# Kernel tuning notes

Measured on AMD Instinct MI355X. Metric: run time of the kernel, lower is better.

## Reference

```python
import jax, jax.numpy as jnp
import numpy as np

B, S, D = 128, 256, 768          # batch, seq (pre-sentinel), encoder dim
ARC, TAG = 500, 100              # arc / tag representation dims
LAYERS, TOPK = 2, 8              # config['gnn_layers'], config['top_k']
SP = S + 1                       # seq_len after head sentinel


def setup_inputs() -> dict:
    key = jax.random.key(0)
    ks = jax.random.split(key, 32)
    sc = 0.02
    inp = {
        'inputs': jax.random.normal(ks[0], (B, S, D), jnp.float32),
        'tag_embeddings': jax.random.randint(ks[1], (B, S), 0, 50),
        'mask': jnp.ones((B, S), jnp.int32),
        'head_indices': jax.random.randint(ks[2], (B, S), 0, S),
        'head_tags': jax.random.randint(ks[3], (B, S), 0, 50),
        # parameters
        'head_sentinel': jax.random.normal(ks[4], (D,), jnp.float32),
        'W_ha': jax.random.normal(ks[5], (D, ARC)) * sc, 'b_ha': jnp.zeros((ARC,)),
        'W_da': jax.random.normal(ks[6], (D, ARC)) * sc, 'b_da': jnp.zeros((ARC,)),
        'W_ht': jax.random.normal(ks[7], (D, TAG)) * sc, 'b_ht': jnp.zeros((TAG,)),
        'W_dt': jax.random.normal(ks[8], (D, TAG)) * sc, 'b_dt': jnp.zeros((TAG,)),
        # bilinear attention: use_input_biases=True -> (ARC+1, ARC+1), plus scalar bias
        'bil_W': jax.random.normal(ks[9], (LAYERS + 1, ARC + 1, ARC + 1)) * sc,
        'bil_b': jnp.zeros((LAYERS + 1,)),
        # GCNConv params (PyG: x @ W, symmetric-normalized aggregate, + bias)
        'c1a_W': jax.random.normal(ks[10], (ARC, ARC)) * sc, 'c1a_b': jnp.zeros((ARC,)),
        'c2a_W': jax.random.normal(ks[11], (ARC, ARC)) * sc, 'c2a_b': jnp.zeros((ARC,)),
        'c1r_W': jax.random.normal(ks[12], (TAG, TAG)) * sc, 'c1r_b': jnp.zeros((TAG,)),
        'c2r_W': jax.random.normal(ks[13], (TAG, TAG)) * sc, 'c2r_b': jnp.zeros((TAG,)),
    }
    return inp


def bilinear_attn(m1, m2, W, b):
    # AllenNLP BilinearMatrixAttention with use_input_biases=True
    ones1 = jnp.ones(m1.shape[:-1] + (1,), m1.dtype)
    m1b = jnp.concatenate([m1, ones1], -1)
    m2b = jnp.concatenate([m2, ones1], -1)
    return jnp.einsum('bie,ef,bjf->bij', m1b, W, m2b) + b


def batch_top_k(probs, k):
    # probs: [B, SP, SP] row-softmaxed; edge j(head)->i(dep) for each row's top-k cols,
    # with global (batched) node indexing.
    vals, idx = jax.lax.top_k(probs, k)                      # [B, SP, k]
    offs = (jnp.arange(B) * SP)[:, None, None]
    src = (idx + offs).reshape(-1)
    dst = (jnp.broadcast_to(jnp.arange(SP)[None, :, None], idx.shape) + offs).reshape(-1)
    return src, dst, vals.reshape(-1)


def gcn_conv(x, src, dst, ew, W, b):
    # PyG GCNConv: x@W, add self-loops (weight 1), sym norm, scatter-add at dst, + bias
    N = x.shape[0]
    x = x @ W
    loop = jnp.arange(N)
    row = jnp.concatenate([src, loop])
    col = jnp.concatenate([dst, loop])
    w = jnp.concatenate([ew, jnp.ones((N,), x.dtype)])
    deg = jax.ops.segment_sum(w, col, num_segments=N)
    dinv = jnp.where(deg > 0, jax.lax.rsqrt(deg), 0.0)
    norm = dinv[row] * w * dinv[col]
    out = jax.ops.segment_sum(x[row] * norm[:, None], col, num_segments=N)
    return out + b


def reference(inputs, tag_embeddings, mask, head_indices, head_tags,
              head_sentinel, W_ha, b_ha, W_da, b_da, W_ht, b_ht, W_dt, b_dt,
              bil_W, bil_b, c1a_W, c1a_b, c2a_W, c2a_b, c1r_W, c1r_b, c2r_W, c2r_b):
    elu = jax.nn.elu
    x = jnp.concatenate([jnp.broadcast_to(head_sentinel, (B, 1, D)), inputs], axis=1)  # [B,SP,D]
    head_arc = elu(x @ W_ha + b_ha)
    dept_arc = elu(x @ W_da + b_da)
    head_tag = elu(x @ W_ht + b_ht)
    dep_tag = elu(x @ W_dt + b_dt)

    def two_conv(feat, W1, b1, W2, b2, src, dst, ew):
        h = gcn_conv(feat.reshape(B * SP, -1), src, dst, ew, W1, b1)
        h = gcn_conv(elu(h), src, dst, ew, W2, b2)
        return h.reshape(B, SP, -1)

    for k in range(LAYERS):
        arc_logits = bilinear_attn(head_arc, dept_arc, bil_W[k], bil_b[k])
        arc_probs = jax.nn.softmax(arc_logits, axis=-1)
        src, dst, ew = batch_top_k(arc_probs, TOPK)
        head_arc = two_conv(head_arc, c1a_W, c1a_b, c2a_W, c2a_b, src, dst, ew)
        dept_arc = two_conv(dept_arc, c1a_W, c1a_b, c2a_W, c2a_b, src, dst, ew)
        head_tag = two_conv(head_tag, c1r_W, c1r_b, c2r_W, c2r_b, src, dst, ew)
        dep_tag = two_conv(dep_tag, c1r_W, c1r_b, c2r_W, c2r_b, src, dst, ew)

    arc_logits = bilinear_attn(head_arc, dept_arc, bil_W[-1], bil_b[-1])
    return arc_logits, head_tag, dep_tag
```

## Files before the change

### kernel.cpp

```cpp
#include <hip/hip_runtime.h>
#include <hip/hip_bf16.h>
#include <math.h>
#include <cstddef>

namespace {

constexpr int kB   = 128;
constexpr int kS   = 256;
constexpr int kD   = 768;
constexpr int kSP  = 257;
constexpr int kN   = kB * kSP;
constexpr int kARC = 500;
constexpr int kTAG = 100;
constexpr int KA   = 512;
constexpr int KT   = 128;
constexpr int NPA  = 1024;
constexpr int NPT  = 256;

typedef __attribute__((ext_vector_type(8))) short short8;
typedef __attribute__((ext_vector_type(4))) float floatx4;
typedef __attribute__((ext_vector_type(2))) float floatx2;
typedef __attribute__((ext_vector_type(4))) unsigned short ushort4v;
typedef __attribute__((ext_vector_type(2))) unsigned short ushort2v;
typedef __hip_bfloat16 bf;

__device__ __forceinline__ float bfval(bf h) { return __bfloat162float(h); }
__device__ __forceinline__ unsigned short bfbits(bf h) {
  unsigned short u; __builtin_memcpy(&u, &h, 2); return u;
}
__device__ __forceinline__ void splitf(float x, bf* h, bf* l) {
  bf hh = __float2bfloat16(x);
  *h = hh;
  *l = __float2bfloat16(x - __bfloat162float(hh));
}

__device__ __forceinline__ int swz8(int lid, int total) {
  int q = total >> 3, r = total & 7;
  int c = lid & 7, p = lid >> 3;
  return (c < r ? c * (q + 1) : r * (q + 1) + (c - r) * q) + p;
}

__device__ __forceinline__ void gload16(const bf* g, bf* l) {
  __builtin_amdgcn_global_load_lds(
      (const __attribute__((address_space(1))) void*)g,
      (__attribute__((address_space(3))) void*)l, 16, 0, 0);
}

__global__ void zerofill(unsigned* __restrict__ p, long n4) {
  long i = (long)blockIdx.x * 256 + threadIdx.x;
  if (i < n4) p[i] = 0u;
}

__global__ void detect_dtype_n(const unsigned* __restrict__ raw, int* __restrict__ flag,
                               int nwords) {
  int lane = threadIdx.x;
  int ok = 0, nz = 0;
  if (lane < nwords) {
    unsigned w = raw[lane];
    if (w != 0u) {
      nz = 1;
      int e = (w >> 7) & 0xFF;
      ok = (e >= 90 && e <= 140);
    }
  }
  unsigned long long ball_ok = __ballot(ok);
  unsigned long long ball_nz = __ballot(nz);
  if (lane == 0) {
    int cok = __popcll(ball_ok), cnz = __popcll(ball_nz);
    flag[0] = (cok * 4 >= cnz * 3) ? 1 : 0;
  }
}

__device__ __forceinline__ float rawload(const void* p, size_t i, int bfm) {
  return bfm ? __bfloat162float(((const bf*)p)[i]) : ((const float*)p)[i];
}

__global__ void conv_off(const void* __restrict__ src, float* __restrict__ dst,
                         int n, long off, const int* __restrict__ flag) {
  int i = blockIdx.x * 256 + threadIdx.x;
  if (i >= n) return;
  dst[i] = rawload(src, (size_t)off + i, *flag);
}

__global__ void wsplit_t(const void* __restrict__ src, const int* __restrict__ flag,
                         long srcOff, int ldsrc, int K, int N, int Kpad,
                         bf* __restrict__ Wh, bf* __restrict__ Wl) {
  long idx = (long)blockIdx.x * 256 + threadIdx.x;
  if (idx >= (long)N * Kpad) return;
  int n = (int)(idx / Kpad), k = (int)(idx % Kpad);
  float v = (k < K) ? rawload(src, (size_t)srcOff + (size_t)k * ldsrc + n, *flag) : 0.f;
  bf h, l;
  splitf(v, &h, &l);
  Wh[idx] = h; Wl[idx] = l;
}

__global__ void xsplit(const void* __restrict__ inp, const void* __restrict__ sent,
                       const int* __restrict__ fi, const int* __restrict__ fs,
                       bf* __restrict__ xh, bf* __restrict__ xl, int g0, int NG) {
  long idx = (long)blockIdx.x * 256 + threadIdx.x;
  long tot = (long)NG * (kD / 4);
  if (idx >= tot) return;
  int n = (int)(idx / (kD / 4));
  int k = (int)(idx % (kD / 4)) * 4;
  int b = n / kSP, r = n - b * kSP;
  const void* src;
  size_t base;
  int bfm;
  if (r == 0) { src = sent; base = (size_t)k; bfm = *fs; }
  else {
    src = inp;
    base = ((size_t)((g0 + b) * kS + (r - 1))) * kD + k;
    bfm = *fi;
  }
  float v[4];
  if (bfm) {
    ushort4v s = *(const ushort4v*)((const unsigned short*)src + base);
#pragma unroll
    for (int j = 0; j < 4; ++j) {
      bf h; unsigned short u = s[j];
      __builtin_memcpy(&h, &u, 2);
      v[j] = __bfloat162float(h);
    }
  } else {
    floatx4 f4 = *(const floatx4*)((const float*)src + base);
#pragma unroll
    for (int j = 0; j < 4; ++j) v[j] = f4[j];
  }
  ushort4v h4, l4;
#pragma unroll
  for (int j = 0; j < 4; ++j) {
    bf h, l;
    splitf(v[j], &h, &l);
    h4[j] = bfbits(h); l4[j] = bfbits(l);
  }
  size_t o = (size_t)n * kD + k;
  *(ushort4v*)((unsigned short*)xh + o) = h4;
  *(ushort4v*)((unsigned short*)xl + o) = l4;
}

constexpr int BM = 128, BN = 128, BK = 32;

template <int EPI, int OUTF32>
__global__ __launch_bounds__(256) void gemm_sp(
    const bf* __restrict__ Ah, const bf* __restrict__ Al, int lda,
    const bf* __restrict__ Bh, const bf* __restrict__ Bl, int ldb,
    bf* __restrict__ Ch, bf* __restrict__ Cl, float* __restrict__ Cf, int ldc,
    int M, int N, int K, const float* __restrict__ bias) {
  __shared__ bf sAh[2][BM][BK];
  __shared__ bf sAl[2][BM][BK];
  __shared__ bf sBh[2][BN][BK];
  __shared__ bf sBl[2][BN][BK];
  const int tid = threadIdx.x;
  const int lane = tid & 63, wave = tid >> 6;
  const int quad = lane >> 4, l15 = lane & 15;
  const int wm = (wave >> 1) * 64, wn = (wave & 1) * 64;
  const int gy = gridDim.y;
  const int sw = swz8(blockIdx.x + blockIdx.y * gridDim.x, gridDim.x * gy);
  const int m0 = (sw / gy) * BM, n0 = (sw % gy) * BN;
  const int lrow = lane >> 2, lkof = (lane & 3) * 8;

  const bf *pAh[2], *pAl[2], *pBh[2], *pBl[2];
  int rb[2];
#pragma unroll
  for (int jj = 0; jj < 2; ++jj) {
    rb[jj] = wave * 32 + jj * 16;
    int gm = m0 + rb[jj] + lrow; if (gm > M - 1) gm = M - 1;
    int gn = n0 + rb[jj] + lrow; if (gn > N - 1) gn = N - 1;
    pAh[jj] = Ah + (size_t)gm * lda + lkof;
    pAl[jj] = Al + (size_t)gm * lda + lkof;
    pBh[jj] = Bh + (size_t)gn * ldb + lkof;
    pBl[jj] = Bl + (size_t)gn * ldb + lkof;
  }

  auto stage = [&](int bi, int k0) {
#pragma unroll
    for (int jj = 0; jj < 2; ++jj) {
      gload16(pAh[jj] + k0, &sAh[bi][rb[jj]][0]);
      gload16(pAl[jj] + k0, &sAl[bi][rb[jj]][0]);
      gload16(pBh[jj] + k0, &sBh[bi][rb[jj]][0]);
      gload16(pBl[jj] + k0, &sBl[bi][rb[jj]][0]);
    }
  };

  floatx4 acc[4][4] = {};
  stage(0, 0);
  int cur = 0;
  for (int k0 = 0; k0 < K; k0 += BK) {
    __syncthreads();
    if (k0 + BK < K) stage(cur ^ 1, k0 + BK);
    short8 a_h[4], a_l[4], b_h[4], b_l[4];
#pragma unroll
    for (int t = 0; t < 4; ++t) {
      a_h[t] = *(const short8*)&sAh[cur][wm + t * 16 + l15][quad * 8];
      a_l[t] = *(const short8*)&sAl[cur][wm + t * 16 + l15][quad * 8];
      b_h[t] = *(const short8*)&sBh[cur][wn + t * 16 + l15][quad * 8];
      b_l[t] = *(const short8*)&sBl[cur][wn + t * 16 + l15][quad * 8];
    }
#pragma unroll
    for (int mt = 0; mt < 4; ++mt)
#pragma unroll
      for (int nt = 0; nt < 4; ++nt) {
        acc[mt][nt] = __builtin_amdgcn_mfma_f32_16x16x32_bf16(a_h[mt], b_h[nt], acc[mt][nt], 0, 0, 0);
        acc[mt][nt] = __builtin_amdgcn_mfma_f32_16x16x32_bf16(a_h[mt], b_l[nt], acc[mt][nt], 0, 0, 0);
        acc[mt][nt] = __builtin_amdgcn_mfma_f32_16x16x32_bf16(a_l[mt], b_h[nt], acc[mt][nt], 0, 0, 0);
      }
    cur ^= 1;
  }
#pragma unroll
  for (int mt = 0; mt < 4; ++mt)
#pragma unroll
    for (int reg = 0; reg < 4; ++reg) {
      int m = m0 + wm + mt * 16 + quad * 4 + reg;
      if (m >= M) continue;
#pragma unroll
      for (int nt = 0; nt < 4; ++nt) {
        int n = n0 + wn + nt * 16 + l15;
        if (OUTF32) {
          if (n < N) {
            float v = acc[mt][nt][reg];
            if (EPI >= 1) v += bias[n];
            if (EPI == 1) v = v > 0.f ? v : expm1f(v);
            Cf[(size_t)m * ldc + n] = v;
          }
        } else {
          size_t o = (size_t)m * ldc + n;
          if (n < N) {
            float v = acc[mt][nt][reg];
            if (EPI >= 1) v += bias[n];
            if (EPI == 1) v = v > 0.f ? v : expm1f(v);
            bf h, l;
            splitf(v, &h, &l);
            Ch[o] = h; Cl[o] = l;
          } else if (n < ldc) {
            Ch[o] = __float2bfloat16(0.f);
            Cl[o] = __float2bfloat16(0.f);
          }
        }
      }
    }
}

__global__ __launch_bounds__(256) void bilnt_sp(
    const bf* __restrict__ Th, const bf* __restrict__ Tl,
    const bf* __restrict__ Fh, const bf* __restrict__ Fl, int ldf,
    float* __restrict__ out, const float* __restrict__ bilb, int bidx,
    int g0, int globOut) {
  __shared__ bf sAh[2][BM][BK];
  __shared__ bf sAl[2][BM][BK];
  __shared__ bf sBh[2][BN][BK];
  __shared__ bf sBl[2][BN][BK];
  const int tid = threadIdx.x;
  const int lane = tid & 63, wave = tid >> 6;
  const int quad = lane >> 4, l15 = lane & 15;
  const int wm = (wave >> 1) * 64, wn = (wave & 1) * 64;
  const int gx = gridDim.x, gxy = gridDim.x * gridDim.y;
  const int sw = swz8(blockIdx.x + gx * blockIdx.y + gxy * blockIdx.z, gxy * gridDim.z);
  const int z = sw / gxy;
  const int rem = sw % gxy;
  const int m0 = (rem % gx) * BM, n0 = (rem / gx) * BN;
  const int lrow = lane >> 2, lkof = (lane & 3) * 8;
  const bf* Ah = Th + (size_t)z * kSP * KA;
  const bf* Al = Tl + (size_t)z * kSP * KA;
  const bf* Bh = Fh + (size_t)z * kSP * ldf;
  const bf* Bl = Fl + (size_t)z * kSP * ldf;

  const bf *pAh[2], *pAl[2], *pBh[2], *pBl[2];
  int rb[2];
#pragma unroll
  for (int jj = 0; jj < 2; ++jj) {
    rb[jj] = wave * 32 + jj * 16;
    int gm = m0 + rb[jj] + lrow; if (gm > kSP - 1) gm = kSP - 1;
    int gn = n0 + rb[jj] + lrow; if (gn > kSP - 1) gn = kSP - 1;
    pAh[jj] = Ah + (size_t)gm * KA + lkof;
    pAl[jj] = Al + (size_t)gm * KA + lkof;
    pBh[jj] = Bh + (size_t)gn * ldf + lkof;
    pBl[jj] = Bl + (size_t)gn * ldf + lkof;
  }

  auto stage = [&](int bi, int k0) {
#pragma unroll
    for (int jj = 0; jj < 2; ++jj) {
      gload16(pAh[jj] + k0, &sAh[bi][rb[jj]][0]);
      gload16(pAl[jj] + k0, &sAl[bi][rb[jj]][0]);
      gload16(pBh[jj] + k0, &sBh[bi][rb[jj]][0]);
      gload16(pBl[jj] + k0, &sBl[bi][rb[jj]][0]);
    }
  };

  floatx4 acc[4][4] = {};
  stage(0, 0);
  int cur = 0;
  for (int k0 = 0; k0 < KA; k0 += BK) {
    __syncthreads();
    if (k0 + BK < KA) stage(cur ^ 1, k0 + BK);
    short8 a_h[4], a_l[4], b_h[4], b_l[4];
#pragma unroll
    for (int t = 0; t < 4; ++t) {
      a_h[t] = *(const short8*)&sAh[cur][wm + t * 16 + l15][quad * 8];
      a_l[t] = *(const short8*)&sAl[cur][wm + t * 16 + l15][quad * 8];
      b_h[t] = *(const short8*)&sBh[cur][wn + t * 16 + l15][quad * 8];
      b_l[t] = *(const short8*)&sBl[cur][wn + t * 16 + l15][quad * 8];
    }
#pragma unroll
    for (int mt = 0; mt < 4; ++mt)
#pragma unroll
      for (int nt = 0; nt < 4; ++nt) {
        acc[mt][nt] = __builtin_amdgcn_mfma_f32_16x16x32_bf16(a_h[mt], b_h[nt], acc[mt][nt], 0, 0, 0);
        acc[mt][nt] = __builtin_amdgcn_mfma_f32_16x16x32_bf16(a_h[mt], b_l[nt], acc[mt][nt], 0, 0, 0);
        acc[mt][nt] = __builtin_amdgcn_mfma_f32_16x16x32_bf16(a_l[mt], b_h[nt], acc[mt][nt], 0, 0, 0);
      }
    cur ^= 1;
  }
  const float sb = bilb[bidx];
  const int bb = globOut ? (g0 + z) : z;
#pragma unroll
  for (int mt = 0; mt < 4; ++mt)
#pragma unroll
    for (int reg = 0; reg < 4; ++reg) {
      int i = m0 + wm + mt * 16 + quad * 4 + reg;
      if (i >= kSP) continue;
      float rowterm = bfval(Ah[(size_t)i * KA + 500]) + bfval(Al[(size_t)i * KA + 500]) + sb;
#pragma unroll
      for (int nt = 0; nt < 4; ++nt) {
        int j = n0 + wn + nt * 16 + l15;
        if (j >= kSP) continue;
        out[((size_t)bb * kSP + i) * kSP + j] = acc[mt][nt][reg] + rowterm;
      }
    }
}

__global__ void softmax_topk(const float* __restrict__ logits,
                             int* __restrict__ idx8,
                             float* __restrict__ val8,
                             float* __restrict__ dinv) {
  const int row = blockIdx.x;
  const int lane = threadIdx.x;
  const int rowbase = row - (row % kSP);
  const float* L = logits + (size_t)row * kSP;
  float v[5];
  int c[5];
#pragma unroll
  for (int q = 0; q < 5; ++q) {
    int j = lane + q * 64;
    c[q] = j;
    v[q] = (j < kSP) ? L[j] : -INFINITY;
  }
  float m = v[0];
#pragma unroll
  for (int q = 1; q < 5; ++q) m = fmaxf(m, v[q]);
  for (int off = 32; off > 0; off >>= 1) m = fmaxf(m, __shfl_xor(m, off));
  float s = 0.f;
#pragma unroll
  for (int q = 0; q < 5; ++q) s += expf(v[q] - m);
  for (int off = 32; off > 0; off >>= 1) s += __shfl_xor(s, off);
  const float invs = 1.f / s;
  float degsum = 0.f;
  for (int t = 0; t < 8; ++t) {
    float bvv = -INFINITY;
    int bii = kSP;
#pragma unroll
    for (int q = 0; q < 5; ++q)
      if (v[q] > bvv) { bvv = v[q]; bii = c[q]; }
    for (int off = 32; off > 0; off >>= 1) {
      float ov = __shfl_xor(bvv, off);
      int oi = __shfl_xor(bii, off);
      if (ov > bvv || (ov == bvv && oi < bii)) { bvv = ov; bii = oi; }
    }
    float p = expf(bvv - m) * invs;
    degsum += p;
    if (lane == 0) { idx8[row * 8 + t] = rowbase + bii; val8[row * 8 + t] = p; }
#pragma unroll
    for (int q = 0; q < 5; ++q)
      if (c[q] == bii) v[q] = -INFINITY;
  }
  if (lane == 0) dinv[row] = 1.f / sqrtf(1.f + degsum);
}

template <int ELU, int OUTF32>
__global__ void gcn_agg(const float* __restrict__ Y, int ldy, int F,
                        const int* __restrict__ idx8, const float* __restrict__ val8,
                        const float* __restrict__ dinv, const float* __restrict__ bias,
                        bf* __restrict__ Zh, bf* __restrict__ Zl,
                        float* __restrict__ Zf, int ldzf, long halfStr) {
  const int r = swz8(blockIdx.x, gridDim.x);
  const int m = r >> 1, p = r & 1;
  __shared__ float w[9];
  __shared__ int srcs[8];
  const int t = threadIdx.x;
  if (t < 8) {
    int s = idx8[m * 8 + t];
    srcs[t] = 2 * s + p;
    w[t] = dinv[m] * val8[m * 8 + t] * dinv[s];
  } else if (t == 8) {
    float di = dinv[m];
    w[8] = di * di;
  }
  __syncthreads();
  const int lim = OUTF32 ? F : ldy;
  for (int f = t * 2; f < lim; f += (int)blockDim.x * 2) {
    size_t on = (size_t)r * ldy + f;
    if (!OUTF32 && f >= F) {
      ushort2v zz = {0, 0};
      *(ushort2v*)((unsigned short*)Zh + on) = zz;
      *(ushort2v*)((unsigned short*)Zl + on) = zz;
      continue;
    }
    floatx2 y0 = *(const floatx2*)(Y + on);
    float a0 = w[8] * y0[0], a1 = w[8] * y0[1];
#pragma unroll
    for (int e = 0; e < 8; ++e) {
      floatx2 ys = *(const floatx2*)(Y + (size_t)srcs[e] * ldy + f);
      a0 += w[e] * ys[0];
      a1 += w[e] * ys[1];
    }
    a0 += bias[f];
    a1 += bias[f + 1];
    if (ELU) {
      a0 = a0 > 0.f ? a0 : expm1f(a0);
      a1 = a1 > 0.f ? a1 : expm1f(a1);
    }
    if (OUTF32) {
      float* zp = Zf + (size_t)p * halfStr + (size_t)m * ldzf + f;
      floatx2 o = {a0, a1};
      *(floatx2*)zp = o;
    } else {
      bf h0, l0, h1, l1;
      splitf(a0, &h0, &l0);
      splitf(a1, &h1, &l1);
      ushort2v hv = {bfbits(h0), bfbits(h1)};
      ushort2v lv = {bfbits(l0), bfbits(l1)};
      *(ushort2v*)((unsigned short*)Zh + on) = hv;
      *(ushort2v*)((unsigned short*)Zl + on) = lv;
    }
  }
}

}

extern "C" void kernel_launch(void* const* d_in, const int* in_sizes, int n_in,
                              void* d_out, int out_size, void* d_ws, size_t ws_size,
                              hipStream_t stream) {
  (void)out_size;

  const int roleSize[20] = {kB * kS * kD, kD,
                            kD * kARC, kARC, kD * kARC, kARC,
                            kD * kTAG, kTAG, kD * kTAG, kTAG,
                            3 * 501 * 501, 3,
                            kARC * kARC, kARC, kARC * kARC, kARC,
                            kTAG * kTAG, kTAG, kTAG * kTAG, kTAG};
  const int roleOcc[20]  = {0, 0, 0, 0, 1, 1, 0, 0, 1, 1, 0, 0,
                            0, 2, 1, 3, 0, 2, 1, 3};
  int roleIdx[20] = {0, 5, 6, 7, 8, 9, 10, 11, 12, 13, 14, 15,
                     16, 17, 18, 19, 20, 21, 22, 23};
  for (int r = 0; r < 20; ++r) {
    int occ = 0, found = -1;
    for (int i = 0; i < n_in; ++i) {
      if (in_sizes[i] == roleSize[r]) {
        if (occ == roleOcc[r]) { found = i; break; }
        ++occ;
      }
    }
    if (found >= 0) roleIdx[r] = found;
    else if (roleIdx[r] >= n_in) roleIdx[r] = 0;
  }
  const void* src_of[20];
  for (int r = 0; r < 20; ++r) src_of[r] = d_in[roleIdx[r]];

  auto need_bytes = [](int GB) -> size_t {
    size_t NG = (size_t)GB * kSP, s = 0;
    auto al = [&](size_t b) { s += (b + 255) & ~(size_t)255; };
    al(256);
    al((size_t)NPA * kD * 2); al((size_t)NPA * kD * 2);
    al((size_t)NPT * kD * 2); al((size_t)NPT * kD * 2);
    al(NPA * 4); al(NPT * 4);
    for (int i = 0; i < 6; ++i) al((size_t)501 * KA * 2);
    al(3 * 501 * 4); al(256);
    for (int i = 0; i < 4; ++i) al((size_t)kARC * KA * 2);
    for (int i = 0; i < 4; ++i) al((size_t)kTAG * KT * 2);
    al(kARC * 4); al(kARC * 4); al(kTAG * 4); al(kTAG * 4);
    al(NG * kD * 2); al(NG * kD * 2);
    al(NG * NPA * 2); al(NG * NPA * 2);
    al(NG * NPT * 2); al(NG * NPT * 2);
    al(NG * KA * 2); al(NG * KA * 2);
    al(NG * NPA * 2); al(NG * NPA * 2);
    al(NG * NPA * 4);
    al(NG * kSP * 4);
    al(NG * 8 * 4); al(NG * 8 * 4); al(NG * 4);
    return s;
  };
  int GB = 1;
  for (int cand : {128, 64, 32, 16, 8, 4, 2, 1})
    if (need_bytes(cand) <= ws_size) { GB = cand; break; }
  const int G = kB / GB;
  const int NG = GB * kSP;
  const int mb  = (NG + BM - 1) / BM;
  const int mb2 = (2 * NG + BM - 1) / BM;

  char* ws = (char*)d_ws;
  size_t off = 0;
  auto alloc = [&](size_t bytes) -> void* {
    void* p = ws + off;
    off += (bytes + 255) & ~(size_t)255;
    return p;
  };
  int* flags = (int*)alloc(256);
  bf *WtABh = (bf*)alloc((size_t)NPA * kD * 2), *WtABl = (bf*)alloc((size_t)NPA * kD * 2);
  bf *WtTBh = (bf*)alloc((size_t)NPT * kD * 2), *WtTBl = (bf*)alloc((size_t)NPT * kD * 2);
  float* bpa = (float*)alloc(NPA * 4);
  float* bpt = (float*)alloc(NPT * 4);
  bf* bilWh[3]; bf* bilWl[3];
  for (int k = 0; k < 3; ++k) {
    bilWh[k] = (bf*)alloc((size_t)501 * KA * 2);
    bilWl[k] = (bf*)alloc((size_t)501 * KA * 2);
  }
  float* brow = (float*)alloc(3 * 501 * 4);
  float* bilbf = (float*)alloc(256);
  bf *c1ah = (bf*)alloc((size_t)kARC * KA * 2), *c1al = (bf*)alloc((size_t)kARC * KA * 2);
  bf *c2ah = (bf*)alloc((size_t)kARC * KA * 2), *c2al = (bf*)alloc((size_t)kARC * KA * 2);
  bf *c1rh = (bf*)alloc((size_t)kTAG * KT * 2), *c1rl = (bf*)alloc((size_t)kTAG * KT * 2);
  bf *c2rh = (bf*)alloc((size_t)kTAG * KT * 2), *c2rl = (bf*)alloc((size_t)kTAG * KT * 2);
  float* c1ab = (float*)alloc(kARC * 4);
  float* c2ab = (float*)alloc(kARC * 4);
  float* c1rb = (float*)alloc(kTAG * 4);
  float* c2rb = (float*)alloc(kTAG * 4);
  bf *xh = (bf*)alloc((size_t)NG * kD * 2), *xl = (bf*)alloc((size_t)NG * kD * 2);
  bf *FAh = (bf*)alloc((size_t)NG * NPA * 2), *FAl = (bf*)alloc((size_t)NG * NPA * 2);
  bf *FTh = (bf*)alloc((size_t)NG * NPT * 2), *FTl = (bf*)alloc((size_t)NG * NPT * 2);
  bf *Th = (bf*)alloc((size_t)NG * KA * 2), *Tl = (bf*)alloc((size_t)NG * KA * 2);
  bf *Z2h = (bf*)alloc((size_t)NG * NPA * 2), *Z2l = (bf*)alloc((size_t)NG * NPA * 2);
  float* Yf = (float*)alloc((size_t)NG * NPA * 4);
  float* logits = (float*)alloc((size_t)NG * kSP * 4);
  int*   idx8 = (int*)alloc((size_t)NG * 8 * 4);
  float* val8 = (float*)alloc((size_t)NG * 8 * 4);
  float* dinv = (float*)alloc((size_t)NG * 4);

  for (int r = 0; r < 20; ++r) {
    int n = roleSize[r];
    int nwords = n / 4; if (nwords < 1) nwords = 1; if (nwords > 64) nwords = 64;
    detect_dtype_n<<<1, 64, 0, stream>>>((const unsigned*)src_of[r], flags + r, nwords);
  }
  auto cvt = [&](int role, float* dst, int n, long o) {
    conv_off<<<(n + 255) / 256, 256, 0, stream>>>(src_of[role], dst, n, o, flags + role);
  };
  auto wsp = [&](int role, long o, int ldsrc, int K, int N, int Kpad, bf* Wh, bf* Wl) {
    long tot = (long)N * Kpad;
    wsplit_t<<<(int)((tot + 255) / 256), 256, 0, stream>>>(src_of[role], flags + role, o,
                                                           ldsrc, K, N, Kpad, Wh, Wl);
  };
  auto zf = [&](void* p, size_t bytes) {
    long n4 = (long)(bytes / 4);
    zerofill<<<(int)((n4 + 255) / 256), 256, 0, stream>>>((unsigned*)p, n4);
  };

  zf(WtABh, (size_t)NPA * kD * 2); zf(WtABl, (size_t)NPA * kD * 2);
  zf(WtTBh, (size_t)NPT * kD * 2); zf(WtTBl, (size_t)NPT * kD * 2);
  zf(bpa, NPA * 4); zf(bpt, NPT * 4);
  wsp(2, 0, kARC, kD, kARC, kD, WtABh, WtABl);
  wsp(4, 0, kARC, kD, kARC, kD, WtABh + (size_t)KA * kD, WtABl + (size_t)KA * kD);
  wsp(6, 0, kTAG, kD, kTAG, kD, WtTBh, WtTBl);
  wsp(8, 0, kTAG, kD, kTAG, kD, WtTBh + (size_t)KT * kD, WtTBl + (size_t)KT * kD);
  cvt(3, bpa, kARC, 0); cvt(5, bpa + KA, kARC, 0);
  cvt(7, bpt, kTAG, 0); cvt(9, bpt + KT, kTAG, 0);
  cvt(11, bilbf, 3, 0);
  cvt(13, c1ab, kARC, 0); cvt(15, c2ab, kARC, 0); cvt(17, c1rb, kTAG, 0); cvt(19, c2rb, kTAG, 0);
  for (int k = 0; k < 3; ++k) {
    wsp(10, (long)k * 501 * 501, 501, 500, 501, KA, bilWh[k], bilWl[k]);
    cvt(10, brow + k * 501, 501, (long)k * 501 * 501 + 500 * 501);
  }
  wsp(12, 0, kARC, kARC, kARC, KA, c1ah, c1al);
  wsp(14, 0, kARC, kARC, kARC, KA, c2ah, c2al);
  wsp(16, 0, kTAG, kTAG, kTAG, KT, c1rh, c1rl);
  wsp(18, 0, kTAG, kTAG, kTAG, KT, c2rh, c2rl);

  float* outp = (float*)d_out;
  const size_t arc_elems = (size_t)kB * kSP * kSP;

  for (int g = 0; g < G; ++g) {
    const int g0 = g * GB;

    {
      long tot = (long)NG * (kD / 4);
      xsplit<<<(int)((tot + 255) / 256), 256, 0, stream>>>(
          src_of[0], src_of[1], flags + 0, flags + 1, xh, xl, g0, NG);
    }
    gemm_sp<1, 0><<<dim3(mb, NPA / BN), 256, 0, stream>>>(
        xh, xl, kD, WtABh, WtABl, kD, FAh, FAl, nullptr, NPA, NG, NPA, kD, bpa);
    gemm_sp<1, 0><<<dim3(mb, NPT / BN), 256, 0, stream>>>(
        xh, xl, kD, WtTBh, WtTBl, kD, FTh, FTl, nullptr, NPT, NG, NPT, kD, bpt);

    for (int k = 0; k < 2; ++k) {
      gemm_sp<2, 0><<<dim3(mb, 4), 256, 0, stream>>>(
          FAh, FAl, NPA, bilWh[k], bilWl[k], KA, Th, Tl, nullptr, KA, NG, 501, KA,
          brow + k * 501);
      bilnt_sp<<<dim3(3, 3, GB), 256, 0, stream>>>(
          Th, Tl, FAh + KA, FAl + KA, NPA, logits, bilbf, k, g0, 0);
      softmax_topk<<<NG, 64, 0, stream>>>(logits, idx8, val8, dinv);

      gemm_sp<0, 1><<<dim3(mb2, 4), 256, 0, stream>>>(
          FAh, FAl, KA, c1ah, c1al, KA, nullptr, nullptr, Yf, KA, 2 * NG, kARC, KA, nullptr);
      gcn_agg<1, 0><<<2 * NG, 256, 0, stream>>>(Yf, KA, kARC, idx8, val8, dinv, c1ab,
                                                Z2h, Z2l, nullptr, 0, 0);
      gemm_sp<0, 1><<<dim3(mb2, 4), 256, 0, stream>>>(
          Z2h, Z2l, KA, c2ah, c2al, KA, nullptr, nullptr, Yf, KA, 2 * NG, kARC, KA, nullptr);
      gcn_agg<0, 0><<<2 * NG, 256, 0, stream>>>(Yf, KA, kARC, idx8, val8, dinv, c2ab,
                                                FAh, FAl, nullptr, 0, 0);

      gemm_sp<0, 1><<<dim3(mb2, 1), 256, 0, stream>>>(
          FTh, FTl, KT, c1rh, c1rl, KT, nullptr, nullptr, Yf, KT, 2 * NG, kTAG, KT, nullptr);
      gcn_agg<1, 0><<<2 * NG, 64, 0, stream>>>(Yf, KT, kTAG, idx8, val8, dinv, c1rb,
                                               Z2h, Z2l, nullptr, 0, 0);
      gemm_sp<0, 1><<<dim3(mb2, 1), 256, 0, stream>>>(
          Z2h, Z2l, KT, c2rh, c2rl, KT, nullptr, nullptr, Yf, KT, 2 * NG, kTAG, KT, nullptr);
      if (k == 1) {
        float* dst = outp + arc_elems + (size_t)g0 * kSP * kTAG;
        gcn_agg<0, 1><<<2 * NG, 64, 0, stream>>>(Yf, KT, kTAG, idx8, val8, dinv, c2rb,
                                                 nullptr, nullptr, dst, kTAG,
                                                 (long)kN * kTAG);
      } else {
        gcn_agg<0, 0><<<2 * NG, 64, 0, stream>>>(Yf, KT, kTAG, idx8, val8, dinv, c2rb,
                                                 FTh, FTl, nullptr, 0, 0);
      }
    }

    gemm_sp<2, 0><<<dim3(mb, 4), 256, 0, stream>>>(
        FAh, FAl, NPA, bilWh[2], bilWl[2], KA, Th, Tl, nullptr, KA, NG, 501, KA,
        brow + 2 * 501);
    bilnt_sp<<<dim3(3, 3, GB), 256, 0, stream>>>(
        Th, Tl, FAh + KA, FAl + KA, NPA, outp, bilbf, 2, g0, 1);
  }
}
```

Baseline: 2.798 ms.

## Alias workspace buffers and shrink top-k indices to allow larger batch groups

```diff
diff --git a/kernel.cpp b/kernel.cpp
--- a/kernel.cpp
+++ b/kernel.cpp
@@ -330,12 +330,11 @@
 }
 
 __global__ void softmax_topk(const float* __restrict__ logits,
-                             int* __restrict__ idx8,
+                             unsigned short* __restrict__ idx8,
                              float* __restrict__ val8,
                              float* __restrict__ dinv) {
   const int row = blockIdx.x;
   const int lane = threadIdx.x;
-  const int rowbase = row - (row % kSP);
   const float* L = logits + (size_t)row * kSP;
   float v[5];
   int c[5];
@@ -357,7 +356,7 @@
   float degsum = 0.f;
   for (int t = 0; t < 8; ++t) {
     float bvv = -INFINITY;
-    int bii = kSP;
+    int bii = 0;
 #pragma unroll
     for (int q = 0; q < 5; ++q)
       if (v[q] > bvv) { bvv = v[q]; bii = c[q]; }
@@ -368,7 +367,7 @@
     }
     float p = expf(bvv - m) * invs;
     degsum += p;
-    if (lane == 0) { idx8[row * 8 + t] = rowbase + bii; val8[row * 8 + t] = p; }
+    if (lane == 0) { idx8[row * 8 + t] = (unsigned short)bii; val8[row * 8 + t] = p; }
 #pragma unroll
     for (int q = 0; q < 5; ++q)
       if (c[q] == bii) v[q] = -INFINITY;
@@ -378,7 +377,8 @@
 
 template <int ELU, int OUTF32>
 __global__ void gcn_agg(const float* __restrict__ Y, int ldy, int F,
-                        const int* __restrict__ idx8, const float* __restrict__ val8,
+                        const unsigned short* __restrict__ idx8,
+                        const float* __restrict__ val8,
                         const float* __restrict__ dinv, const float* __restrict__ bias,
                         bf* __restrict__ Zh, bf* __restrict__ Zl,
                         float* __restrict__ Zf, int ldzf, long halfStr) {
@@ -388,7 +388,8 @@
   __shared__ int srcs[8];
   const int t = threadIdx.x;
   if (t < 8) {
-    int s = idx8[m * 8 + t];
+    int b0 = m - (m % kSP);
+    int s = b0 + (int)idx8[m * 8 + t];
     srcs[t] = 2 * s + p;
     w[t] = dinv[m] * val8[m * 8 + t] * dinv[s];
   } else if (t == 8) {
@@ -466,7 +467,14 @@
   const void* src_of[20];
   for (int r = 0; r < 20; ++r) src_of[r] = d_in[roleIdx[r]];
 
-  auto need_bytes = [](int GB) -> size_t {
+  auto r1_bytes = [](size_t NG) -> size_t {
+    size_t a = (size_t)2 * NG * KA * 4;
+    size_t b = NG * kD * 2 * 2;
+    size_t c = NG * KA * 2 * 2 + NG * kSP * 4;
+    size_t m = a; if (b > m) m = b; if (c > m) m = c;
+    return m;
+  };
+  auto need_bytes = [&](int GB) -> size_t {
     size_t NG = (size_t)GB * kSP, s = 0;
     auto al = [&](size_t b) { s += (b + 255) & ~(size_t)255; };
     al(256);
@@ -478,14 +486,11 @@
     for (int i = 0; i < 4; ++i) al((size_t)kARC * KA * 2);
     for (int i = 0; i < 4; ++i) al((size_t)kTAG * KT * 2);
     al(kARC * 4); al(kARC * 4); al(kTAG * 4); al(kTAG * 4);
-    al(NG * kD * 2); al(NG * kD * 2);
     al(NG * NPA * 2); al(NG * NPA * 2);
     al(NG * NPT * 2); al(NG * NPT * 2);
-    al(NG * KA * 2); al(NG * KA * 2);
-    al(NG * NPA * 2); al(NG * NPA * 2);
-    al(NG * NPA * 4);
-    al(NG * kSP * 4);
-    al(NG * 8 * 4); al(NG * 8 * 4); al(NG * 4);
+    al(r1_bytes(NG));
+    al((size_t)2 * NG * KA * 2 * 2);
+    al(NG * 8 * 2); al(NG * 8 * 4); al(NG * 4);
     return s;
   };
   int GB = 1;
@@ -523,14 +528,18 @@
   float* c2ab = (float*)alloc(kARC * 4);
   float* c1rb = (float*)alloc(kTAG * 4);
   float* c2rb = (float*)alloc(kTAG * 4);
-  bf *xh = (bf*)alloc((size_t)NG * kD * 2), *xl = (bf*)alloc((size_t)NG * kD * 2);
   bf *FAh = (bf*)alloc((size_t)NG * NPA * 2), *FAl = (bf*)alloc((size_t)NG * NPA * 2);
   bf *FTh = (bf*)alloc((size_t)NG * NPT * 2), *FTl = (bf*)alloc((size_t)NG * NPT * 2);
-  bf *Th = (bf*)alloc((size_t)NG * KA * 2), *Tl = (bf*)alloc((size_t)NG * KA * 2);
-  bf *Z2h = (bf*)alloc((size_t)NG * NPA * 2), *Z2l = (bf*)alloc((size_t)NG * NPA * 2);
-  float* Yf = (float*)alloc((size_t)NG * NPA * 4);
-  float* logits = (float*)alloc((size_t)NG * kSP * 4);
-  int*   idx8 = (int*)alloc((size_t)NG * 8 * 4);
+  char* R1 = (char*)alloc(r1_bytes((size_t)NG));
+  bf* xh = (bf*)R1;
+  bf* xl = xh + (size_t)NG * kD;
+  bf* Th = (bf*)R1;
+  bf* Tl = Th + (size_t)NG * KA;
+  float* logits = (float*)(R1 + (size_t)NG * KA * 2 * 2);
+  float* Yf = (float*)R1;
+  bf* Z2h = (bf*)alloc((size_t)2 * NG * KA * 2 * 2);
+  bf* Z2l = Z2h + (size_t)2 * NG * KA;
+  unsigned short* idx8 = (unsigned short*)alloc((size_t)NG * 8 * 2);
   float* val8 = (float*)alloc((size_t)NG * 8 * 4);
   float* dinv = (float*)alloc((size_t)NG * 4);
 
```

Measured after the change: 2.741 ms. -2.0%, faster.
